# Performance work log

Measured on AMD Instinct MI355X. Metric: run time of the kernel, lower is better.

The kernel has to match this reference:

```python
import jax, jax.numpy as jnp
import numpy as np

BIG_NEG = -1.0e6  # constants.big_negative


def setup_inputs() -> dict:
    key = jax.random.key(0)
    ks = jax.random.split(key, 10)
    B, N, NF, HNF, M, T = 2048, 100, 128, 128, 128, 12
    hidden_output_nodes = jax.random.normal(ks[0], (B, N, HNF), dtype=jnp.float32)
    input_nodes = jax.random.normal(ks[1], (B, N, NF), dtype=jnp.float32)
    node_mask = jax.random.uniform(ks[2], (B, N)) < 0.8
    node_mask = node_mask.at[:, 0].set(True)  # avoid fully-masked rows
    s = 0.05
    W_emb = jax.random.normal(ks[3], (M, NF + HNF), dtype=jnp.float32) * s
    b_emb = jnp.zeros((M,), dtype=jnp.float32)
    W_ih = jax.random.normal(ks[4], (4 * M, M), dtype=jnp.float32) * s
    b_ih = jnp.zeros((4 * M,), dtype=jnp.float32)
    W_hh = jax.random.normal(ks[5], (4 * M, M), dtype=jnp.float32) * s
    b_hh = jnp.zeros((4 * M,), dtype=jnp.float32)
    return {
        "hidden_output_nodes": hidden_output_nodes,
        "input_nodes": input_nodes,
        "W_emb": W_emb, "b_emb": b_emb,
        "W_ih": W_ih, "b_ih": b_ih, "W_hh": W_hh, "b_hh": b_hh,
        "node_mask": node_mask,
        "lstm_computations": T,
    }


def _set2vec(hidden_output_nodes, input_nodes, W_emb, b_emb, W_ih, b_ih, W_hh, b_hh, node_mask, T):
    B = input_nodes.shape[0]
    M = W_emb.shape[0]
    # memory: [B, N, M]
    cat = jnp.concatenate((hidden_output_nodes, input_nodes), axis=2)
    memory = jnp.einsum("bnf,mf->bnm", cat, W_emb) + b_emb
    energy_mask = (~node_mask).astype(memory.dtype) * BIG_NEG  # [B, N]

    zeros = jnp.zeros((B, M), dtype=memory.dtype)

    def step(carry, _):
        lstm_in, h, c = carry
        # LSTMCell (PyTorch gate order: i, f, g, o)
        gates = lstm_in @ W_ih.T + b_ih + h @ W_hh.T + b_hh
        i, f, g, o = jnp.split(gates, 4, axis=-1)
        c = jax.nn.sigmoid(f) * c + jax.nn.sigmoid(i) * jnp.tanh(g)
        q = jax.nn.sigmoid(o) * jnp.tanh(c)  # query / new hidden state
        # dot-product attention read over the node memory
        energies = jnp.einsum("bm,bnm->bn", q, memory) + energy_mask
        attn = jax.nn.softmax(energies, axis=1)
        read = jnp.einsum("bn,bnm->bm", attn, memory)
        return (read, q, c), None

    (read, q, _), _ = jax.lax.scan(step, (zeros, zeros, zeros), None, length=T)
    return jnp.concatenate((q, read), axis=1)  # [B, 2*M]


def reference(hidden_output_nodes, input_nodes, W_emb, b_emb, W_ih, b_ih, W_hh, b_hh, node_mask, lstm_computations):
    return _set2vec(hidden_output_nodes, input_nodes, W_emb, b_emb, W_ih, b_ih, W_hh, b_hh, node_mask, lstm_computations)
```

## Files before the change

kernel.cpp:

```cpp
#include <hip/hip_runtime.h>
#include <hip/hip_fp16.h>
#include <math.h>

#define BIG_NEG  (-1.0e6f)
#define NN   100
#define MD   128
#define KD   256
#define G4   512
#define NB   4
#define MP2  68
#define XPAD 288

#define WS_WGF_H  32768
#define WS_BIAS_F 81920

typedef _Float16 f16x2 __attribute__((ext_vector_type(2)));
typedef _Float16 f16x8 __attribute__((ext_vector_type(8)));
typedef float    f32x4 __attribute__((ext_vector_type(4)));

#if __has_builtin(__builtin_amdgcn_rcpf)
#define RCPF(x) __builtin_amdgcn_rcpf(x)
#else
#define RCPF(x) (1.0f / (x))
#endif

#define PKRTZ(a, b) __builtin_bit_cast(unsigned, __builtin_amdgcn_cvt_pkrtz((a), (b)))

__device__ __forceinline__ float sigm(float x) {
    return RCPF(1.0f + __expf(-x));
}
__device__ __forceinline__ float tanh_f(float x) {
    float xc = fminf(fmaxf(x, -15.0f), 15.0f);
    float e  = __expf(2.0f * xc);
    return (e - 1.0f) * RCPF(e + 1.0f);
}

extern "C" __global__ void prep_kernel(const float* __restrict__ W_emb,
                                       const float* __restrict__ W_ih,
                                       const float* __restrict__ b_ih,
                                       const float* __restrict__ W_hh,
                                       const float* __restrict__ b_hh,
                                       float* __restrict__ ws) {
    int tid = blockIdx.x * blockDim.x + threadIdx.x;
    int nth = gridDim.x * blockDim.x;
    __half* WF    = (__half*)ws;
    __half* WG    = (__half*)ws + WS_WGF_H;
    float*  biasc = ws + WS_BIAS_F;
    for (int i = tid; i < 32768; i += nth) {
        int kg = i >> 10, m = (i >> 3) & 127, j = i & 7;
        WF[i] = __float2half(W_emb[m * 256 + kg * 8 + j]);
    }
    for (int i = tid; i < 131072; i += nth) {
        int kc = i >> 12, g = (i >> 3) & 511, j = i & 7;
        int k = kc * 8 + j;
        float w = (k < 128) ? W_ih[g * 128 + k] : W_hh[g * 128 + (k - 128)];
        WG[i] = __float2half(w);
    }
    for (int i = tid; i < 512; i += nth) biasc[i] = b_ih[i] + b_hh[i];
}

extern "C" __global__ __launch_bounds__(1024, 4)
void set2vec_main(const float* __restrict__ hidden,
                  const float* __restrict__ input,
                  const float* __restrict__ b_emb,
                  const unsigned char* __restrict__ mask_bytes,
                  const int* __restrict__ Tptr,
                  const float* __restrict__ ws,
                  float* __restrict__ out) {
    __shared__ __half2 mem2[NB][NN][MP2];
    __shared__ __half  xcath[NB][XPAD];
    __shared__ float   xcat2[NB][KD];
    __shared__ float   cbuf[NB][MD];
    __shared__ float   emask[NB][NN];
    __shared__ float   bbuf[G4];
    __shared__ int     mask_is_u8;
    __shared__ float   gbuf[NB][G4];
    __shared__ float   ebuf[NB][128];
    __shared__ float   abuf[NB][NN];

    const int tid  = threadIdx.x;
    const int b0   = blockIdx.x * NB;
    const int lane = tid & 63, wv = tid >> 6;
    const int ln15 = lane & 15, lhi = lane >> 4;
    const __half* WF   = (const __half*)ws;
    const __half* memh = (const __half*)mem2;

    if (tid == 0) {
        int nz = 0;
        for (int i = 0; i < 64; ++i)
            if ((i & 3) && mask_bytes[i]) nz = 1;
        mask_is_u8 = nz;
    }

    {
        const float be0 = b_emb[0 * 16 + ln15], be1 = b_emb[1 * 16 + ln15];
        const float be2 = b_emb[2 * 16 + ln15], be3 = b_emb[3 * 16 + ln15];
        const float be4 = b_emb[4 * 16 + ln15], be5 = b_emb[5 * 16 + ln15];
        const float be6 = b_emb[6 * 16 + ln15], be7 = b_emb[7 * 16 + ln15];
        __half* memw = (__half*)mem2;
        for (int tile = wv; tile < 25; tile += 16) {
            f32x4 acc0 = {be0, be0, be0, be0}, acc1 = {be1, be1, be1, be1};
            f32x4 acc2 = {be2, be2, be2, be2}, acc3 = {be3, be3, be3, be3};
            f32x4 acc4 = {be4, be4, be4, be4}, acc5 = {be5, be5, be5, be5};
            f32x4 acc6 = {be6, be6, be6, be6}, acc7 = {be7, be7, be7, be7};

            const int rA     = tile * 16 + ln15;
            const int rAok   = rA < NB * NN;
            const long gbase = ((long)(b0 * NN + rA)) << 7;

            #pragma unroll 1
            for (int mk = 0; mk < 8; ++mk) {
                f16x8 aF;
                if (rAok) {
                    int k0 = mk * 32 + lhi * 8;
                    const float* src = (k0 < 128) ? (hidden + gbase + k0)
                                                  : (input + gbase + (k0 - 128));
                    float4 v0 = *(const float4*)src;
                    float4 v1 = *(const float4*)(src + 4);
                    union { f16x8 v; unsigned u[4]; } au;
                    au.u[0] = PKRTZ(v0.x, v0.y);
                    au.u[1] = PKRTZ(v0.z, v0.w);
                    au.u[2] = PKRTZ(v1.x, v1.y);
                    au.u[3] = PKRTZ(v1.z, v1.w);
                    aF = au.v;
                } else {
                    aF = (f16x8)(_Float16)0.0f;
                }
                const __half* wrow = WF + ((mk * 4 + lhi) * 128 + ln15) * 8;
#define EMB_CT(CT, ACC) { \
                union { uint4 u; f16x8 v; } bu; \
                bu.u = *(const uint4*)(wrow + (CT * 16) * 8); \
                ACC = __builtin_amdgcn_mfma_f32_16x16x32_f16(aF, bu.v, ACC, 0, 0, 0); }
                EMB_CT(0, acc0) EMB_CT(1, acc1) EMB_CT(2, acc2) EMB_CT(3, acc3)
                EMB_CT(4, acc4) EMB_CT(5, acc5) EMB_CT(6, acc6) EMB_CT(7, acc7)
#undef EMB_CT
            }
#define EMB_WR(CT, ACC) { \
            _Pragma("unroll") \
            for (int reg = 0; reg < 4; ++reg) { \
                int r = tile * 16 + lhi * 4 + reg; \
                if (r < NB * NN) { \
                    int bb = r / NN, n = r - (r / NN) * NN; \
                    memw[(bb * NN + n) * (2 * MP2) + CT * 16 + ln15] = __float2half(ACC[reg]); \
                } } }
            EMB_WR(0, acc0) EMB_WR(1, acc1) EMB_WR(2, acc2) EMB_WR(3, acc3)
            EMB_WR(4, acc4) EMB_WR(5, acc5) EMB_WR(6, acc6) EMB_WR(7, acc7)
#undef EMB_WR
        }
    }

    const uint4* WgB = (const uint4*)((const __half*)ws + WS_WGF_H);
    const int ct0 = wv * 2, ct1 = wv * 2 + 1;
#define LDW(KS) \
    const uint4 wA##KS = WgB[((KS) * 4 + lhi) * 512 + ct0 * 16 + ln15]; \
    const uint4 wB##KS = WgB[((KS) * 4 + lhi) * 512 + ct1 * 16 + ln15];
    LDW(0) LDW(1) LDW(2) LDW(3) LDW(4) LDW(5) LDW(6) LDW(7)
#undef LDW

    for (int i = tid; i < NB * XPAD; i += 1024) ((__half*)xcath)[i] = __float2half(0.0f);
    ((float*)xcat2)[tid] = 0.0f;
    if (tid < NB * MD) ((float*)cbuf)[tid] = 0.0f;
    if (tid < G4) bbuf[tid] = ws[WS_BIAS_F + tid];
    if (tid < NB * NN) {
        int bb = tid / NN, n = tid - bb * NN;
        long mrow = (long)(b0 + bb) * NN + n;
        int valid = mask_is_u8 ? (mask_bytes[mrow] != 0)
                               : (((const int*)mask_bytes)[mrow] != 0);
        emask[bb][n] = valid ? 0.0f : BIG_NEG;
    }
    __syncthreads();

    const int T = Tptr[0];

    const __half* aBase = &xcath[ln15 & 3][lhi * 8];

    const int ep0 = wv * 2, ep1 = wv * 2 + 1;
    const int e_bb0 = ep0 / 7, e_nt0 = ep0 - e_bb0 * 7;
    const int e_bb1 = ep1 / 7, e_nt1 = ep1 - e_bb1 * 7;
    const int e_n0  = e_nt0 * 16 + ln15, e_n1 = e_nt1 * 16 + ln15;
    const int e_n0c = (e_n0 < 100) ? e_n0 : 99;
    const int e_n1c = (e_n1 < 100) ? e_n1 : 99;
    const __half* eB0 = memh + (e_bb0 * NN + e_n0c) * (2 * MP2) + lhi * 8;
    const __half* eB1 = memh + (e_bb1 * NN + e_n1c) * (2 * MP2) + lhi * 8;
    const __half* eA0 = &xcath[e_bb0][128 + lhi * 8];
    const __half* eA1 = &xcath[e_bb1][128 + lhi * 8];

    const int r_s = lane >> 2, r_nq = lane & 3;
    const __half* rBase = memh + (wv & 3) * NN * (2 * MP2) + r_s * 8;

    for (int step = 0; step < T; ++step) {
        {
            f32x4 ga = {0.f, 0.f, 0.f, 0.f}, gb = {0.f, 0.f, 0.f, 0.f};
#define GS(KS) { \
            union { uint4 u; f16x8 v; } a, ba, bc; \
            a.u  = *(const uint4*)(aBase + (KS) * 32); \
            ba.u = wA##KS; bc.u = wB##KS; \
            ga = __builtin_amdgcn_mfma_f32_16x16x32_f16(a.v, ba.v, ga, 0, 0, 0); \
            gb = __builtin_amdgcn_mfma_f32_16x16x32_f16(a.v, bc.v, gb, 0, 0, 0); }
            GS(0) GS(1) GS(2) GS(3) GS(4) GS(5) GS(6) GS(7)
#undef GS
            if (lhi == 0) {
                #pragma unroll
                for (int r = 0; r < 4; ++r) {
                    gbuf[r][ct0 * 16 + ln15] = ga[r];
                    gbuf[r][ct1 * 16 + ln15] = gb[r];
                }
            }
        }
        __syncthreads();
        if (tid < NB * MD) {
            int bb = tid >> 7, m = tid & 127;
            float gi = gbuf[bb][m]       + bbuf[m];
            float gf = gbuf[bb][128 + m] + bbuf[128 + m];
            float gg = gbuf[bb][256 + m] + bbuf[256 + m];
            float go = gbuf[bb][384 + m] + bbuf[384 + m];
            float c  = cbuf[bb][m];
            c = sigm(gf) * c + sigm(gi) * tanh_f(gg);
            float qv = sigm(go) * tanh_f(c);
            cbuf[bb][m] = c;
            xcat2[bb][128 + m] = qv;
            xcath[bb][128 + m] = __float2half(qv);
        }
        __syncthreads();
        if (wv < 14) {
            f32x4 e0 = {0.f, 0.f, 0.f, 0.f}, e1 = {0.f, 0.f, 0.f, 0.f};
#define ES(KS) { \
            union { uint4 u; f16x8 v; } a0, a1, bq0, bq1; \
            a0.u  = *(const uint4*)(eA0 + (KS) * 32); \
            bq0.u = *(const uint4*)(eB0 + (KS) * 32); \
            a1.u  = *(const uint4*)(eA1 + (KS) * 32); \
            bq1.u = *(const uint4*)(eB1 + (KS) * 32); \
            e0 = __builtin_amdgcn_mfma_f32_16x16x32_f16(a0.v, bq0.v, e0, 0, 0, 0); \
            e1 = __builtin_amdgcn_mfma_f32_16x16x32_f16(a1.v, bq1.v, e1, 0, 0, 0); }
            ES(0) ES(1) ES(2) ES(3)
#undef ES
            if (lhi == 0) {
                if (e_n0 < 100) ebuf[e_bb0][e_n0] = e0[0];
                if (e_n1 < 100) ebuf[e_bb1][e_n1] = e1[0];
            }
        }
        __syncthreads();
        if (tid < 256) {
            int bb = tid >> 6, l = tid & 63;
            float e0 = ebuf[bb][l] + emask[bb][l];
            float e1 = -INFINITY;
            if (l < 36) e1 = ebuf[bb][l + 64] + emask[bb][l + 64];
            float mx = fmaxf(e0, e1);
            for (int off = 32; off; off >>= 1) mx = fmaxf(mx, __shfl_xor(mx, off, 64));
            float p0 = __expf(e0 - mx);
            float p1 = (l < 36) ? __expf(e1 - mx) : 0.0f;
            float s = p0 + p1;
            for (int off = 32; off; off >>= 1) s += __shfl_xor(s, off, 64);
            float inv = RCPF(s);
            abuf[bb][l] = p0 * inv;
            if (l < 36) abuf[bb][l + 64] = p1 * inv;
        }
        __syncthreads();
        if (tid < 256) {
            int bb = wv & 3;
            float a0 = 0.f, a1 = 0.f, a2 = 0.f, a3 = 0.f;
            float a4 = 0.f, a5 = 0.f, a6 = 0.f, a7 = 0.f;
            #pragma unroll 5
            for (int j = 0; j < 25; ++j) {
                int n = r_nq * 25 + j;
                float av = abuf[bb][n];
                uint4 u  = *(const uint4*)(rBase + n * (2 * MP2));
                float2 f0 = __half22float2(*(__half2*)&u.x);
                float2 f1 = __half22float2(*(__half2*)&u.y);
                float2 f2 = __half22float2(*(__half2*)&u.z);
                float2 f3 = __half22float2(*(__half2*)&u.w);
                a0 = fmaf(av, f0.x, a0); a1 = fmaf(av, f0.y, a1);
                a2 = fmaf(av, f1.x, a2); a3 = fmaf(av, f1.y, a3);
                a4 = fmaf(av, f2.x, a4); a5 = fmaf(av, f2.y, a5);
                a6 = fmaf(av, f3.x, a6); a7 = fmaf(av, f3.y, a7);
            }
#define RED(A) A += __shfl_xor(A, 1, 64); A += __shfl_xor(A, 2, 64);
            RED(a0) RED(a1) RED(a2) RED(a3) RED(a4) RED(a5) RED(a6) RED(a7)
#undef RED
            if (r_nq == 0) {
                int m = r_s * 8;
                float4 lo = {a0, a1, a2, a3}, hi = {a4, a5, a6, a7};
                *(float4*)&xcat2[bb][m]     = lo;
                *(float4*)&xcat2[bb][m + 4] = hi;
                uint4 hv;
                hv.x = PKRTZ(a0, a1);
                hv.y = PKRTZ(a2, a3);
                hv.z = PKRTZ(a4, a5);
                hv.w = PKRTZ(a6, a7);
                *(uint4*)&xcath[bb][m] = hv;
            }
        }
        __syncthreads();
    }

    {
        int bb = tid >> 8, j = tid & 255;
        float v = (j < 128) ? xcat2[bb][128 + j] : xcat2[bb][j - 128];
        out[((long)(b0 + bb) << 8) + j] = v;
    }
}

extern "C" void kernel_launch(void* const* d_in, const int* in_sizes, int n_in,
                              void* d_out, int out_size, void* d_ws, size_t ws_size,
                              hipStream_t stream) {
    const float* hidden = (const float*)d_in[0];
    const float* input  = (const float*)d_in[1];
    const float* W_emb  = (const float*)d_in[2];
    const float* b_emb  = (const float*)d_in[3];
    const float* W_ih   = (const float*)d_in[4];
    const float* b_ih   = (const float*)d_in[5];
    const float* W_hh   = (const float*)d_in[6];
    const float* b_hh   = (const float*)d_in[7];
    const unsigned char* mask = (const unsigned char*)d_in[8];
    const int*  Tptr    = (const int*)d_in[9];
    float* ws   = (float*)d_ws;
    float* outp = (float*)d_out;

    hipLaunchKernelGGL(prep_kernel, dim3(128), dim3(256), 0, stream,
                       W_emb, W_ih, b_ih, W_hh, b_hh, ws);
    hipLaunchKernelGGL(set2vec_main, dim3(512), dim3(1024), 0, stream,
                       hidden, input, b_emb, mask, Tptr, ws, outp);
}
```

Measured before the change: 171.9 us.

## Fuse softmax into attention read per wave, dropping a barrier and widening the read to 8 waves

```diff
diff --git a/kernel.cpp b/kernel.cpp
--- a/kernel.cpp
+++ b/kernel.cpp
@@ -185,8 +185,11 @@
     const __half* eA0 = &xcath[e_bb0][128 + lhi * 8];
     const __half* eA1 = &xcath[e_bb1][128 + lhi * 8];
 
-    const int r_s = lane >> 2, r_nq = lane & 3;
-    const __half* rBase = memh + (wv & 3) * NN * (2 * MP2) + r_s * 8;
+    const int sr_bb = (wv >> 1) & 3, sr_mh = wv & 1;
+    const int rg = lane >> 3, rs = lane & 7;
+    const int r_start = (rg <= 4) ? rg * 13 : 64 + (rg - 5) * 12;
+    const int r_cnt   = (rg < 4) ? 13 : 12;
+    const __half* rB = memh + sr_bb * NN * (2 * MP2) + sr_mh * 64 + rs * 8;
 
     for (int step = 0; step < T; ++step) {
         {
@@ -235,59 +238,57 @@
             ES(0) ES(1) ES(2) ES(3)
 #undef ES
             if (lhi == 0) {
-                if (e_n0 < 100) ebuf[e_bb0][e_n0] = e0[0];
-                if (e_n1 < 100) ebuf[e_bb1][e_n1] = e1[0];
+                if (e_n0 < 100) ebuf[e_bb0][e_n0] = e0[0] + emask[e_bb0][e_n0];
+                if (e_n1 < 100) ebuf[e_bb1][e_n1] = e1[0] + emask[e_bb1][e_n1];
             }
         }
         __syncthreads();
-        if (tid < 256) {
-            int bb = tid >> 6, l = tid & 63;
-            float e0 = ebuf[bb][l] + emask[bb][l];
-            float e1 = -INFINITY;
-            if (l < 36) e1 = ebuf[bb][l + 64] + emask[bb][l + 64];
-            float mx = fmaxf(e0, e1);
-            for (int off = 32; off; off >>= 1) mx = fmaxf(mx, __shfl_xor(mx, off, 64));
-            float p0 = __expf(e0 - mx);
-            float p1 = (l < 36) ? __expf(e1 - mx) : 0.0f;
-            float s = p0 + p1;
-            for (int off = 32; off; off >>= 1) s += __shfl_xor(s, off, 64);
-            float inv = RCPF(s);
-            abuf[bb][l] = p0 * inv;
-            if (l < 36) abuf[bb][l + 64] = p1 * inv;
-        }
-        __syncthreads();
-        if (tid < 256) {
-            int bb = wv & 3;
+        if (wv < 8) {
+            {
+                float e0 = ebuf[sr_bb][lane];
+                float e1 = (lane < 36) ? ebuf[sr_bb][64 + lane] : -INFINITY;
+                float mx = fmaxf(e0, e1);
+                for (int off = 32; off; off >>= 1) mx = fmaxf(mx, __shfl_xor(mx, off, 64));
+                float p0 = __expf(e0 - mx);
+                float p1 = (lane < 36) ? __expf(e1 - mx) : 0.0f;
+                float s = p0 + p1;
+                for (int off = 32; off; off >>= 1) s += __shfl_xor(s, off, 64);
+                float inv = RCPF(s);
+                abuf[sr_bb][lane] = p0 * inv;
+                if (lane < 36) abuf[sr_bb][64 + lane] = p1 * inv;
+            }
             float a0 = 0.f, a1 = 0.f, a2 = 0.f, a3 = 0.f;
             float a4 = 0.f, a5 = 0.f, a6 = 0.f, a7 = 0.f;
-            #pragma unroll 5
-            for (int j = 0; j < 25; ++j) {
-                int n = r_nq * 25 + j;
-                float av = abuf[bb][n];
-                uint4 u  = *(const uint4*)(rBase + n * (2 * MP2));
-                float2 f0 = __half22float2(*(__half2*)&u.x);
-                float2 f1 = __half22float2(*(__half2*)&u.y);
-                float2 f2 = __half22float2(*(__half2*)&u.z);
-                float2 f3 = __half22float2(*(__half2*)&u.w);
-                a0 = fmaf(av, f0.x, a0); a1 = fmaf(av, f0.y, a1);
-                a2 = fmaf(av, f1.x, a2); a3 = fmaf(av, f1.y, a3);
-                a4 = fmaf(av, f2.x, a4); a5 = fmaf(av, f2.y, a5);
-                a6 = fmaf(av, f3.x, a6); a7 = fmaf(av, f3.y, a7);
-            }
-#define RED(A) A += __shfl_xor(A, 1, 64); A += __shfl_xor(A, 2, 64);
+            #pragma unroll
+            for (int j = 0; j < 13; ++j) {
+                if (j < r_cnt) {
+                    int n = r_start + j;
+                    float av = abuf[sr_bb][n];
+                    uint4 u  = *(const uint4*)(rB + n * (2 * MP2));
+                    float2 f0 = __half22float2(*(__half2*)&u.x);
+                    float2 f1 = __half22float2(*(__half2*)&u.y);
+                    float2 f2 = __half22float2(*(__half2*)&u.z);
+                    float2 f3 = __half22float2(*(__half2*)&u.w);
+                    a0 = fmaf(av, f0.x, a0); a1 = fmaf(av, f0.y, a1);
+                    a2 = fmaf(av, f1.x, a2); a3 = fmaf(av, f1.y, a3);
+                    a4 = fmaf(av, f2.x, a4); a5 = fmaf(av, f2.y, a5);
+                    a6 = fmaf(av, f3.x, a6); a7 = fmaf(av, f3.y, a7);
+                }
+            }
+#define RED(A) A += __shfl_xor(A, 8, 64); A += __shfl_xor(A, 16, 64); A += __shfl_xor(A, 32, 64);
             RED(a0) RED(a1) RED(a2) RED(a3) RED(a4) RED(a5) RED(a6) RED(a7)
 #undef RED
-            if (r_nq == 0) {
-                int m = r_s * 8;
+            if (lane < 8) {
+                int m = sr_mh * 64 + lane * 8;
                 float4 lo = {a0, a1, a2, a3}, hi = {a4, a5, a6, a7};
-                *(float4*)&xcat2[bb][m]     = lo;
-                *(float4*)&xcat2[bb][m + 4] = hi;
+                *(float4*)&xcat2[sr_bb][m]     = lo;
+                *(float4*)&xcat2[sr_bb][m + 4] = hi;
                 uint4 hv;
                 hv.x = PKRTZ(a0, a1);
                 hv.y = PKRTZ(a2, a3);
                 hv.z = PKRTZ(a4, a5);
                 hv.w = PKRTZ(a6, a7);
-                *(uint4*)&xcath[bb][m] = hv;
+                *(uint4*)&xcath[sr_bb][m] = hv;
             }
         }
         __syncthreads();
```

New measurement: 165.5 us. -3.7%, faster.
